# Optimization experiments

Hardware: AMD Instinct MI355X
Metric: run time of the kernel (lower is better)

The kernel has to match this reference:

```python
import jax, jax.numpy as jnp
from jax import lax
import numpy as np

B, T, H, K = 128, 256, 768, 64


def setup_inputs() -> dict:
    key = jax.random.key(0)
    k1, k2, k3, k4 = jax.random.split(key, 4)
    hidden = jax.random.normal(k1, (B, T, H), dtype=jnp.float32)
    masks = jnp.ones((B, T), dtype=jnp.int32)
    target = jax.random.randint(k2, (B, T), 0, K, dtype=jnp.int32)
    W = jax.random.normal(k3, (H, K), dtype=jnp.float32) * 0.02
    b = jnp.zeros((K,), dtype=jnp.float32)
    transitions = jax.random.uniform(k4, (K, K), dtype=jnp.float32)
    return {"hidden": hidden, "masks": masks, "target": target,
            "W": W, "b": b, "transitions": transitions}


def _crf_log_norm(emissions, trans, seq_len):
    # emissions: [B,T,K]; forward algorithm (log-sum-exp recurrence over time)
    Tn = emissions.shape[1]
    alpha0 = emissions[:, 0]  # [B,K]

    def step(alpha, xs):
        emis_t, t = xs
        new = jax.nn.logsumexp(alpha[:, :, None] + trans[None], axis=1) + emis_t
        alpha = jnp.where((t < seq_len)[:, None], new, alpha)
        return alpha, None

    xs = (jnp.swapaxes(emissions[:, 1:], 0, 1), jnp.arange(1, Tn))
    alpha, _ = lax.scan(step, alpha0, xs)
    return jax.nn.logsumexp(alpha, axis=1)  # [B]


def _crf_sequence_score(emissions, tags, trans, seq_len):
    Tn = emissions.shape[1]
    t_idx = jnp.arange(Tn)
    valid = t_idx[None, :] < seq_len[:, None]  # [B,T]
    unary = jnp.take_along_axis(emissions, tags[..., None], axis=2)[..., 0]
    unary = jnp.sum(jnp.where(valid, unary, 0.0), axis=1)
    pair = trans[tags[:, :-1], tags[:, 1:]]  # [B,T-1]
    valid_pair = t_idx[1:][None, :] < seq_len[:, None]
    binary = jnp.sum(jnp.where(valid_pair, pair, 0.0), axis=1)
    return unary + binary


def _crf_decode(emissions, trans, seq_len):
    # Viterbi with backpointers; padded steps carry state (identity backptr)
    Bn, Tn, Kn = emissions.shape
    v0 = emissions[:, 0]

    def step(v, xs):
        emis_t, t = xs
        scores = v[:, :, None] + trans[None]  # [B, K_prev, K_cur]
        bp = jnp.argmax(scores, axis=1).astype(jnp.int32)
        new_v = jnp.max(scores, axis=1) + emis_t
        m = (t < seq_len)[:, None]
        v = jnp.where(m, new_v, v)
        bp = jnp.where(m, bp, jnp.arange(Kn, dtype=jnp.int32)[None])
        return v, bp

    xs = (jnp.swapaxes(emissions[:, 1:], 0, 1), jnp.arange(1, Tn))
    v, bps = lax.scan(step, v0, xs)  # bps: [T-1, B, K]
    best_score = jnp.max(v, axis=1)
    last_tag = jnp.argmax(v, axis=1).astype(jnp.int32)

    def back(tag, bp_t):
        prev = jnp.take_along_axis(bp_t, tag[:, None], axis=1)[:, 0]
        return prev, prev

    _, rev_tags = lax.scan(back, last_tag, bps, reverse=True)  # [T-1, B]
    path = jnp.concatenate([rev_tags, last_tag[None]], axis=0)  # [T, B]
    path = jnp.swapaxes(path, 0, 1)  # [B, T]
    valid = jnp.arange(Tn)[None, :] < seq_len[:, None]
    path = jnp.where(valid, path, 0)
    return path, best_score


def reference(hidden, masks, target, W, b, transitions):
    # dense projection (dropout omitted for determinism)
    emissions = jnp.einsum('bth,hk->btk', hidden, W) + b  # [B,T,K]
    seq_len = jnp.sum(masks, axis=1).astype(jnp.int32)
    log_norm = _crf_log_norm(emissions, transitions, seq_len)
    seq_score = _crf_sequence_score(emissions, target, transitions, seq_len)
    log_likelihood = seq_score - log_norm  # [B]
    decode_predict, _crf_scores = _crf_decode(emissions, transitions, seq_len)
    return decode_predict, log_likelihood
```

## Files before the change

kernel.cpp:

```cpp
#include <hip/hip_runtime.h>

#define B_ 128
#define T_ 256
#define H_ 768
#define K_ 64
#define BT_ (B_ * T_)

template <int CTRL>
__device__ __forceinline__ float dpp_mov_f(float x) {
    return __int_as_float(__builtin_amdgcn_update_dpp(
        __float_as_int(x), __float_as_int(x), CTRL, 0xF, 0xF, false));
}
__device__ __forceinline__ float wave_max64(float x) {
    x = fmaxf(x, dpp_mov_f<0x111>(x));
    x = fmaxf(x, dpp_mov_f<0x112>(x));
    x = fmaxf(x, dpp_mov_f<0x114>(x));
    x = fmaxf(x, dpp_mov_f<0x118>(x));
    x = fmaxf(x, dpp_mov_f<0x142>(x));
    x = fmaxf(x, dpp_mov_f<0x143>(x));
    return __int_as_float(__builtin_amdgcn_readlane(__float_as_int(x), 63));
}
__device__ __forceinline__ float readlane0_f(float x) {
    return __int_as_float(__builtin_amdgcn_readfirstlane(__float_as_int(x)));
}
template <int I>
__device__ __forceinline__ float readlane_f(float x) {
    return __int_as_float(__builtin_amdgcn_readlane(__float_as_int(x), I));
}

#define BK_ 32
#define BM_ 64
#define P_ 66
__global__ __launch_bounds__(256) void gemm_emis(const float* __restrict__ hidden,
                                                 const float* __restrict__ W,
                                                 const float* __restrict__ bias,
                                                 float* __restrict__ emis) {
    __shared__ float At[BK_ * P_];

    const int tid = threadIdx.x;
    const int lane = tid & 63;
    const int wc = __builtin_amdgcn_readfirstlane((tid >> 6) * 16);
    const int rowbase = blockIdx.x * BM_;
    const int srow = tid >> 2;
    const int scol = (tid & 3) * 8;

    float acc[16];
#pragma unroll
    for (int c = 0; c < 16; ++c) acc[c] = bias[wc + c];

    float4 pf0 = *(const float4*)&hidden[(size_t)(rowbase + srow) * H_ + scol];
    float4 pf1 = *(const float4*)&hidden[(size_t)(rowbase + srow) * H_ + scol + 4];

    for (int kb = 0; kb < H_ / BK_; ++kb) {
        __syncthreads();
        At[(scol + 0) * P_ + srow] = pf0.x;
        At[(scol + 1) * P_ + srow] = pf0.y;
        At[(scol + 2) * P_ + srow] = pf0.z;
        At[(scol + 3) * P_ + srow] = pf0.w;
        At[(scol + 4) * P_ + srow] = pf1.x;
        At[(scol + 5) * P_ + srow] = pf1.y;
        At[(scol + 6) * P_ + srow] = pf1.z;
        At[(scol + 7) * P_ + srow] = pf1.w;
        __syncthreads();
        if (kb + 1 < H_ / BK_) {
            pf0 = *(const float4*)&hidden[(size_t)(rowbase + srow) * H_ +
                                          (kb + 1) * BK_ + scol];
            pf1 = *(const float4*)&hidden[(size_t)(rowbase + srow) * H_ +
                                          (kb + 1) * BK_ + scol + 4];
        }
        const float* Wk = &W[(kb * BK_) * K_ + wc];
#pragma unroll 8
        for (int h = 0; h < BK_; ++h) {
            float a = At[h * P_ + lane];
            float4 w0 = *(const float4*)&Wk[h * K_ + 0];
            float4 w1 = *(const float4*)&Wk[h * K_ + 4];
            float4 w2 = *(const float4*)&Wk[h * K_ + 8];
            float4 w3 = *(const float4*)&Wk[h * K_ + 12];
            acc[0]  += a * w0.x;  acc[1]  += a * w0.y;
            acc[2]  += a * w0.z;  acc[3]  += a * w0.w;
            acc[4]  += a * w1.x;  acc[5]  += a * w1.y;
            acc[6]  += a * w1.z;  acc[7]  += a * w1.w;
            acc[8]  += a * w2.x;  acc[9]  += a * w2.y;
            acc[10] += a * w2.z;  acc[11] += a * w2.w;
            acc[12] += a * w3.x;  acc[13] += a * w3.y;
            acc[14] += a * w3.z;  acc[15] += a * w3.w;
        }
    }

    float* e = &emis[(size_t)(rowbase + lane) * K_ + wc];
#pragma unroll
    for (int q = 0; q < 4; ++q)
        *(float4*)&e[q * 4] = make_float4(acc[q * 4], acc[q * 4 + 1],
                                          acc[q * 4 + 2], acc[q * 4 + 3]);
}

__global__ __launch_bounds__(128, 1) void crf_kernel(const float* __restrict__ emis,
                                                     const int* __restrict__ masks,
                                                     const int* __restrict__ target,
                                                     const float* __restrict__ trans,
                                                     float* __restrict__ out) {
    __shared__ __align__(16) float ebuf[T_ * K_];
    __shared__ __align__(16) float vbuf[T_ * K_];
    __shared__ float tbuf[K_ * 65];

    const int tid = threadIdx.x;
    const int lane = tid & 63;
    const int b = blockIdx.x;
    const float* eb = emis + (size_t)b * (T_ * K_);

    {
        const float4* src = (const float4*)eb;
        float4* dst = (float4*)ebuf;
#pragma unroll
        for (int k = 0; k < 32; ++k) dst[tid + k * 128] = src[tid + k * 128];
    }
    int sl = 0;
#pragma unroll
    for (int k = 0; k < 4; ++k) sl += masks[b * T_ + lane + k * 64];
#pragma unroll
    for (int m = 32; m; m >>= 1) sl += __shfl_xor(sl, m, 64);
    const int seq_len = sl;
    __syncthreads();

    if (tid < 64) {
        float Ecol[64];
#pragma unroll
        for (int i = 0; i < 64; ++i) Ecol[i] = __expf(trans[i * K_ + lane]);

        float e_c = ebuf[lane];
        float e00 = readlane0_f(e_c);
        float p = __expf(e_c - e00);
        float C = e00;
        float logD0prev = 0.f;
        float e_n = ebuf[K_ + lane];
        float en0 = readlane0_f(e_n);
        float xg = __expf(e_n - en0);

        for (int t = 1; t < T_; ++t) {
            float e_f = (t < T_ - 1) ? ebuf[(t + 1) * K_ + lane] : 0.f;
            float a0 = 0.f, a1 = 0.f, a2 = 0.f, a3 = 0.f;
            float a4 = 0.f, a5 = 0.f, a6 = 0.f, a7 = 0.f;
#define FWD8(base)                                                     \
            a0 = fmaf(readlane_f<base + 0>(p), Ecol[base + 0], a0);    \
            a1 = fmaf(readlane_f<base + 1>(p), Ecol[base + 1], a1);    \
            a2 = fmaf(readlane_f<base + 2>(p), Ecol[base + 2], a2);    \
            a3 = fmaf(readlane_f<base + 3>(p), Ecol[base + 3], a3);    \
            a4 = fmaf(readlane_f<base + 4>(p), Ecol[base + 4], a4);    \
            a5 = fmaf(readlane_f<base + 5>(p), Ecol[base + 5], a5);    \
            a6 = fmaf(readlane_f<base + 6>(p), Ecol[base + 6], a6);    \
            a7 = fmaf(readlane_f<base + 7>(p), Ecol[base + 7], a7);
            FWD8(0) FWD8(8) FWD8(16) FWD8(24) FWD8(32) FWD8(40) FWD8(48) FWD8(56)
#undef FWD8
            float D = ((a0 + a1) + (a2 + a3)) + ((a4 + a5) + (a6 + a7));
            float pnew = D * xg;
            if (t < seq_len) { p = pnew; C += en0 + logD0prev; }
            float D0 = readlane0_f(D);
            logD0prev = __logf(D0);
            float gn = __fdividef(1.f, D0);
            en0 = readlane0_f(e_f);
            xg = __expf(e_f - en0) * gn;
            e_n = e_f;
        }
        float rs = p;
#pragma unroll
        for (int m = 32; m; m >>= 1) rs += __shfl_xor(rs, m, 64);
        float log_norm = C + __logf(rs);

        float sc = 0.f;
#pragma unroll
        for (int k = 0; k < 4; ++k) {
            int t = lane + k * 64;
            if (t < seq_len) {
                int tg = target[b * T_ + t];
                sc += ebuf[t * K_ + tg];
                if (t >= 1) sc += trans[target[b * T_ + t - 1] * K_ + tg];
            }
        }
#pragma unroll
        for (int m = 32; m; m >>= 1) sc += __shfl_xor(sc, m, 64);
        if (lane == 0) out[BT_ + b] = sc - log_norm;
    } else {
        float Tcol[64];
#pragma unroll
        for (int i = 0; i < 64; ++i) Tcol[i] = trans[i * K_ + lane];
        for (int idx = lane; idx < K_ * K_; idx += 64)
            tbuf[(idx >> 6) * 65 + (idx & 63)] = trans[idx];

        float v = ebuf[lane];
        vbuf[lane] = v;
        float e_n = ebuf[K_ + lane];
        for (int t = 1; t < T_; ++t) {
            float e_f = (t < T_ - 1) ? ebuf[(t + 1) * K_ + lane] : 0.f;
            float m0 = -3.4e38f, m1 = -3.4e38f, m2 = -3.4e38f, m3 = -3.4e38f;
#define VITP(macc, i0, i1)                                                \
            {                                                             \
                float x_ = readlane_f<(i0)>(v) + Tcol[(i0)];              \
                float y_ = readlane_f<(i1)>(v) + Tcol[(i1)];              \
                macc = fmaxf(fmaxf(macc, x_), y_);                        \
            }
#define VIT8(base)                                                        \
            VITP(m0, (base) + 0, (base) + 1)                              \
            VITP(m1, (base) + 2, (base) + 3)                              \
            VITP(m2, (base) + 4, (base) + 5)                              \
            VITP(m3, (base) + 6, (base) + 7)
            VIT8(0) VIT8(8) VIT8(16) VIT8(24) VIT8(32) VIT8(40) VIT8(48) VIT8(56)
#undef VIT8
#undef VITP
            float M = fmaxf(fmaxf(m0, m1), fmaxf(m2, m3));
            float vn = M + e_n;
            if (t < seq_len) v = vn;
            vbuf[t * K_ + lane] = v;
            e_n = e_f;
        }

        float M = wave_max64(v);
        unsigned long long ball = __ballot(v >= M);
        int tag = (int)__builtin_ctzll(ball);

        int path[4];
#pragma unroll
        for (int k = 0; k < 4; ++k) path[k] = 0;
        if (lane == ((T_ - 1) & 63)) path[(T_ - 1) >> 6] = tag;

        float vpre = vbuf[(T_ - 2) * K_ + lane];
        for (int t = T_ - 1; t >= 1; --t) {
            float vnext = (t >= 2) ? vbuf[(t - 2) * K_ + lane] : 0.f;
            if (t < seq_len) {
                float s = vpre + tbuf[lane * 65 + tag];
                float Ms = wave_max64(s);
                unsigned long long bl = __ballot(s >= Ms);
                tag = (int)__builtin_ctzll(bl);
            }
            int pidx = t - 1;
            if (lane == (pidx & 63)) path[pidx >> 6] = tag;
            vpre = vnext;
        }
#pragma unroll
        for (int k = 0; k < 4; ++k) {
            int t = lane + k * 64;
            out[b * T_ + t] = (t < seq_len) ? (float)path[k] : 0.f;
        }
    }
}

extern "C" void kernel_launch(void* const* d_in, const int* in_sizes, int n_in,
                              void* d_out, int out_size, void* d_ws, size_t ws_size,
                              hipStream_t stream) {
    const float* hidden = (const float*)d_in[0];
    const int* masks    = (const int*)d_in[1];
    const int* target   = (const int*)d_in[2];
    const float* W      = (const float*)d_in[3];
    const float* bias   = (const float*)d_in[4];
    const float* trans  = (const float*)d_in[5];
    float* out = (float*)d_out;
    float* emis = (float*)d_ws;

    gemm_emis<<<dim3(BT_ / BM_), dim3(256), 0, stream>>>(hidden, W, bias, emis);
    crf_kernel<<<dim3(B_), dim3(128), 0, stream>>>(emis, masks, target, trans, out);
}
```

Before: 372.8 us.

## Store Viterbi backpointers in LDS and pack four batches per CRF block

The Viterbi forward pass now tracks the argmax index alongside the max and writes a byte backpointer per step into shared memory. Backtracking becomes a single LDS lookup per step instead of a recomputed wave max-reduction plus ballot over stored scores. Emissions are read straight from global memory with two-step-ahead prefetch rather than first staged in LDS, and each block now handles four batch elements with 512 threads across 32 blocks. The tie-break order of the argmax may differ from the old first-index rule, and global-load latency now sits on the serial recurrence if the prefetch does not hide it.

Result: slower. 487.7 us (+30.8%).

```diff
diff --git a/kernel.cpp b/kernel.cpp
--- a/kernel.cpp
+++ b/kernel.cpp
@@ -94,50 +94,45 @@
                                           acc[q * 4 + 2], acc[q * 4 + 3]);
 }
 
-__global__ __launch_bounds__(128, 1) void crf_kernel(const float* __restrict__ emis,
+__global__ __launch_bounds__(512, 1) void crf_kernel(const float* __restrict__ emis,
                                                      const int* __restrict__ masks,
                                                      const int* __restrict__ target,
                                                      const float* __restrict__ trans,
                                                      float* __restrict__ out) {
-    __shared__ __align__(16) float ebuf[T_ * K_];
-    __shared__ __align__(16) float vbuf[T_ * K_];
-    __shared__ float tbuf[K_ * 65];
+    __shared__ unsigned char bpbuf[4][T_][K_];
 
     const int tid = threadIdx.x;
     const int lane = tid & 63;
-    const int b = blockIdx.x;
-    const float* eb = emis + (size_t)b * (T_ * K_);
-
-    {
-        const float4* src = (const float4*)eb;
-        float4* dst = (float4*)ebuf;
-#pragma unroll
-        for (int k = 0; k < 32; ++k) dst[tid + k * 128] = src[tid + k * 128];
-    }
+    const int wv = tid >> 6;
+    const int bq = wv & 3;
+    const int role = wv >> 2;
+    const int b = blockIdx.x * 4 + bq;
+    const float* eg = emis + (size_t)b * (T_ * K_);
+
     int sl = 0;
 #pragma unroll
     for (int k = 0; k < 4; ++k) sl += masks[b * T_ + lane + k * 64];
 #pragma unroll
     for (int m = 32; m; m >>= 1) sl += __shfl_xor(sl, m, 64);
     const int seq_len = sl;
-    __syncthreads();
-
-    if (tid < 64) {
+
+    if (role == 0) {
         float Ecol[64];
 #pragma unroll
         for (int i = 0; i < 64; ++i) Ecol[i] = __expf(trans[i * K_ + lane]);
 
-        float e_c = ebuf[lane];
+        float e_c = eg[lane];
         float e00 = readlane0_f(e_c);
         float p = __expf(e_c - e00);
         float C = e00;
         float logD0prev = 0.f;
-        float e_n = ebuf[K_ + lane];
-        float en0 = readlane0_f(e_n);
-        float xg = __expf(e_n - en0);
+        float eN1 = eg[K_ + lane];
+        float en0 = readlane0_f(eN1);
+        float xg = __expf(eN1 - en0);
+        float eP = eg[2 * K_ + lane];
 
         for (int t = 1; t < T_; ++t) {
-            float e_f = (t < T_ - 1) ? ebuf[(t + 1) * K_ + lane] : 0.f;
+            float eQ = (t <= T_ - 3) ? eg[(t + 2) * K_ + lane] : 0.f;
             float a0 = 0.f, a1 = 0.f, a2 = 0.f, a3 = 0.f;
             float a4 = 0.f, a5 = 0.f, a6 = 0.f, a7 = 0.f;
 #define FWD8(base)                                                     \
@@ -157,9 +152,9 @@
             float D0 = readlane0_f(D);
             logD0prev = __logf(D0);
             float gn = __fdividef(1.f, D0);
-            en0 = readlane0_f(e_f);
-            xg = __expf(e_f - en0) * gn;
-            e_n = e_f;
+            en0 = readlane0_f(eP);
+            xg = __expf(eP - en0) * gn;
+            eP = eQ;
         }
         float rs = p;
 #pragma unroll
@@ -172,7 +167,7 @@
             int t = lane + k * 64;
             if (t < seq_len) {
                 int tg = target[b * T_ + t];
-                sc += ebuf[t * K_ + tg];
+                sc += eg[t * K_ + tg];
                 if (t >= 1) sc += trans[target[b * T_ + t - 1] * K_ + tg];
             }
         }
@@ -183,34 +178,39 @@
         float Tcol[64];
 #pragma unroll
         for (int i = 0; i < 64; ++i) Tcol[i] = trans[i * K_ + lane];
-        for (int idx = lane; idx < K_ * K_; idx += 64)
-            tbuf[(idx >> 6) * 65 + (idx & 63)] = trans[idx];
-
-        float v = ebuf[lane];
-        vbuf[lane] = v;
-        float e_n = ebuf[K_ + lane];
+
+        float v = eg[lane];
+        float eU = eg[K_ + lane];
+        float eP = eg[2 * K_ + lane];
+
         for (int t = 1; t < T_; ++t) {
-            float e_f = (t < T_ - 1) ? ebuf[(t + 1) * K_ + lane] : 0.f;
-            float m0 = -3.4e38f, m1 = -3.4e38f, m2 = -3.4e38f, m3 = -3.4e38f;
-#define VITP(macc, i0, i1)                                                \
-            {                                                             \
-                float x_ = readlane_f<(i0)>(v) + Tcol[(i0)];              \
-                float y_ = readlane_f<(i1)>(v) + Tcol[(i1)];              \
-                macc = fmaxf(fmaxf(macc, x_), y_);                        \
-            }
-#define VIT8(base)                                                        \
-            VITP(m0, (base) + 0, (base) + 1)                              \
-            VITP(m1, (base) + 2, (base) + 3)                              \
-            VITP(m2, (base) + 4, (base) + 5)                              \
-            VITP(m3, (base) + 6, (base) + 7)
-            VIT8(0) VIT8(8) VIT8(16) VIT8(24) VIT8(32) VIT8(40) VIT8(48) VIT8(56)
-#undef VIT8
-#undef VITP
-            float M = fmaxf(fmaxf(m0, m1), fmaxf(m2, m3));
-            float vn = M + e_n;
+            float eQ = (t <= T_ - 3) ? eg[(t + 2) * K_ + lane] : 0.f;
+            float m0 = readlane_f<0>(v)  + Tcol[0];  int i0 = 0;
+            float m1 = readlane_f<16>(v) + Tcol[16]; int i1 = 16;
+            float m2 = readlane_f<32>(v) + Tcol[32]; int i2 = 32;
+            float m3 = readlane_f<48>(v) + Tcol[48]; int i3 = 48;
+#define CAND(c, k)                                                         \
+            { float s_ = readlane_f<(c)*16 + (k)>(v) + Tcol[(c)*16 + (k)]; \
+              bool g_ = s_ > m##c;                                         \
+              m##c = g_ ? s_ : m##c;                                       \
+              i##c = g_ ? ((c)*16 + (k)) : i##c; }
+#define CAND4(k) CAND(0, k) CAND(1, k) CAND(2, k) CAND(3, k)
+            CAND4(1)  CAND4(2)  CAND4(3)  CAND4(4)  CAND4(5)
+            CAND4(6)  CAND4(7)  CAND4(8)  CAND4(9)  CAND4(10)
+            CAND4(11) CAND4(12) CAND4(13) CAND4(14) CAND4(15)
+#undef CAND4
+#undef CAND
+            bool g01 = m1 > m0;
+            float mA = g01 ? m1 : m0;  int iA = g01 ? i1 : i0;
+            bool g23 = m3 > m2;
+            float mB = g23 ? m3 : m2;  int iB = g23 ? i3 : i2;
+            bool gAB = mB > mA;
+            float M  = gAB ? mB : mA;  int iF = gAB ? iB : iA;
+
+            float vn = M + eU;
             if (t < seq_len) v = vn;
-            vbuf[t * K_ + lane] = v;
-            e_n = e_f;
+            bpbuf[bq][t][lane] = (unsigned char)iF;
+            eU = eP; eP = eQ;
         }
 
         float M = wave_max64(v);
@@ -222,18 +222,10 @@
         for (int k = 0; k < 4; ++k) path[k] = 0;
         if (lane == ((T_ - 1) & 63)) path[(T_ - 1) >> 6] = tag;
 
-        float vpre = vbuf[(T_ - 2) * K_ + lane];
         for (int t = T_ - 1; t >= 1; --t) {
-            float vnext = (t >= 2) ? vbuf[(t - 2) * K_ + lane] : 0.f;
-            if (t < seq_len) {
-                float s = vpre + tbuf[lane * 65 + tag];
-                float Ms = wave_max64(s);
-                unsigned long long bl = __ballot(s >= Ms);
-                tag = (int)__builtin_ctzll(bl);
-            }
+            if (t < seq_len) tag = (int)bpbuf[bq][t][tag];
             int pidx = t - 1;
             if (lane == (pidx & 63)) path[pidx >> 6] = tag;
-            vpre = vnext;
         }
 #pragma unroll
         for (int k = 0; k < 4; ++k) {
@@ -256,5 +248,5 @@
     float* emis = (float*)d_ws;
 
     gemm_emis<<<dim3(BT_ / BM_), dim3(256), 0, stream>>>(hidden, W, bias, emis);
-    crf_kernel<<<dim3(B_), dim3(128), 0, stream>>>(emis, masks, target, trans, out);
-}
+    crf_kernel<<<dim3(B_ / 4), dim3(512), 0, stream>>>(emis, masks, target, trans, out);
+}
```
